# Optimization experiments

Hardware: AMD Instinct MI355X
Metric: run time of the kernel (lower is better)

Reference implementation:

```python
import jax, jax.numpy as jnp
import numpy as np

L = 16
IN0 = 7  # 3 + 3 + 1 per the torch module
CH = [16, 32, 16]
N = 500000
NEG_SLOPE = 0.2


def setup_inputs() -> dict:
    key = jax.random.key(0)
    ks = jax.random.split(key, 5)
    x = jax.random.normal(ks[0], (N, IN0), dtype=jnp.float32)
    idx = jax.random.randint(ks[1], (N,), 0, L, dtype=jnp.int32)
    # kaiming-uniform-like init scale per layer fan-in
    def init_w(k, shape):
        fan_in = shape[1]
        bound = float(np.sqrt(6.0 / fan_in))
        return jax.random.uniform(k, shape, dtype=jnp.float32, minval=-bound, maxval=bound)
    W0 = init_w(ks[2], (L, IN0, CH[0]))
    W1 = init_w(ks[3], (L, CH[0], CH[1]))
    W2 = init_w(ks[4], (L, CH[1], CH[2]))
    b0 = jnp.zeros((L, CH[0]), dtype=jnp.float32)
    b1 = jnp.zeros((L, CH[1]), dtype=jnp.float32)
    b2 = jnp.zeros((L, CH[2]), dtype=jnp.float32)
    return {"x": x, "idx": idx, "W0": W0, "b0": b0, "W1": W1, "b1": b1, "W2": W2, "b2": b2}


def reference(x, idx, W0, b0, W1, b1, W2, b2):
    # Per-point expert-indexed MLP: h <- LeakyReLU(h @ W[idx] + b[idx]) per layer.
    h = x
    for W, b in ((W0, b0), (W1, b1), (W2, b2)):
        # gather per-point weight [N, in, out] and bias [N, out], vec-mat per point
        h = jax.nn.leaky_relu(
            jnp.einsum("nc,nco->no", h, W[idx]) + b[idx],
            negative_slope=NEG_SLOPE,
        )
    return h
```

## Files before the change

kernel.cpp:

```cpp
#include <hip/hip_runtime.h>
#include <hip/hip_fp16.h>


#define L_EXP 16
#define IN0   7
#define C0    16
#define C1    32
#define C2    16
#define NEG   0.2f
#define BLK   256
#define MPT   4
#define SEGPAD (BLK * MPT)
#define CHUNK  1024
#define NBM    512

#define NW0 (L_EXP * IN0 * C0)
#define NW1 (L_EXP * C0 * C1)
#define NW2 (L_EXP * C1 * C2)
#define NWTOT (NW0 + NW1 + NW2)
#define PREPBLK ((NWTOT + BLK - 1) / BLK)

#define WS_PART  64
#define WB_W0    33792
#define WB_W1    37376
#define WB_W2    53760
#define WS_PERM  18432

__global__ void k_hist(const int* __restrict__ idx, int n, int nblk,
                       int* __restrict__ ws,
                       const float* __restrict__ W0,
                       const float* __restrict__ W1,
                       const float* __restrict__ W2) {
    int t = threadIdx.x;
    if (blockIdx.x >= nblk) {
        int k = (blockIdx.x - nblk) * BLK + t;
        __half* hW0 = (__half*)((char*)ws + WB_W0);
        __half* hW1 = (__half*)((char*)ws + WB_W1);
        __half* hW2 = (__half*)((char*)ws + WB_W2);
        if (k < NW0) hW0[k] = __float2half(W0[k]);
        else if (k < NW0 + NW1) hW1[k - NW0] = __float2half(W1[k - NW0]);
        else if (k < NWTOT) hW2[k - NW0 - NW1] = __float2half(W2[k - NW0 - NW1]);
        return;
    }
    __shared__ int bins[L_EXP];
    if (t < L_EXP) bins[t] = 0;
    __syncthreads();
    int i4 = blockIdx.x * CHUNK + t * 4;
    if (i4 + 3 < n) {
        int4 v = *reinterpret_cast<const int4*>(idx + i4);
        atomicAdd(&bins[v.x & 15], 1);
        atomicAdd(&bins[v.y & 15], 1);
        atomicAdd(&bins[v.z & 15], 1);
        atomicAdd(&bins[v.w & 15], 1);
    } else {
#pragma unroll
        for (int q = 0; q < 4; ++q)
            if (i4 + q < n) atomicAdd(&bins[idx[i4 + q] & 15], 1);
    }
    __syncthreads();
    if (t < L_EXP) ws[WS_PART + t * NBM + blockIdx.x] = bins[t];
}

__global__ void k_scan(int* __restrict__ ws, int nblk) {
    int t = threadIdx.x;
    int e = t >> 6, l = t & 63;
    int running = 0;
    for (int c = 0; c < nblk; c += 64) {
        int b = c + l;
        int v = (b < nblk) ? ws[WS_PART + e * NBM + b] : 0;
        int s = v;
#pragma unroll
        for (int d = 1; d < 64; d <<= 1) {
            int u = __shfl_up(s, d, 64);
            if (l >= d) s += u;
        }
        if (b < nblk) ws[WS_PART + e * NBM + b] = running + (s - v);
        running += __shfl(s, 63, 64);
    }
    if (l == 0) ws[e] = running;
    __syncthreads();
    if (t == 0) {
        int run = 0;
        for (int q = 0; q < L_EXP; ++q) {
            ws[16 + q] = run;
            run += ((ws[q] + SEGPAD - 1) / SEGPAD) * SEGPAD;
        }
        ws[32] = run;
    }
}

__global__ void k_scatter(const int* __restrict__ idx, int n,
                          int* __restrict__ ws) {
    __shared__ int soff[L_EXP];
    __shared__ int lcount[L_EXP];
    int t = threadIdx.x;
    if (t < L_EXP) {
        soff[t] = ws[16 + t] + ws[WS_PART + t * NBM + blockIdx.x];
        lcount[t] = 0;
    }
    __syncthreads();
    int i4 = blockIdx.x * CHUNK + t * 4;
#pragma unroll
    for (int q = 0; q < 4; ++q) {
        int i = i4 + q;
        if (i < n) {
            int e = idx[i] & 15;
            int r = atomicAdd(&lcount[e], 1);
            ws[WS_PERM + soff[e] + r] = i;
        }
    }
}

__device__ __forceinline__ float leaky(float a) { return fmaxf(a, NEG * a); }

__device__ __forceinline__ void h8_unpack(float4 v, float* w) {
    const __half2* p = reinterpret_cast<const __half2*>(&v);
    float2 f0 = __half22float2(p[0]);
    float2 f1 = __half22float2(p[1]);
    float2 f2 = __half22float2(p[2]);
    float2 f3 = __half22float2(p[3]);
    w[0] = f0.x; w[1] = f0.y; w[2] = f1.x; w[3] = f1.y;
    w[4] = f2.x; w[5] = f2.y; w[6] = f3.x; w[7] = f3.y;
}

__global__ void __launch_bounds__(BLK, 2) k_mlp(
    const int* __restrict__ meta, const float* __restrict__ x,
    const float* __restrict__ b0, const float* __restrict__ b1,
    const float* __restrict__ b2, float* __restrict__ out) {
    __shared__ __align__(16) __half sW0h[IN0 * C0];
    __shared__ __align__(16) __half sW1h[C0 * C1];
    __shared__ __align__(16) __half sW2h[C1 * C2];
    __shared__ __align__(16) float sB0[C0];
    __shared__ __align__(16) float sB1[C1];
    __shared__ __align__(16) float sB2[C2];

    int start = blockIdx.x * SEGPAD;
    if (start >= meta[32]) return;

    int e = 0;
    while (start >= meta[16 + e + 1]) ++e;
    e = __builtin_amdgcn_readfirstlane(e);

    int t = threadIdx.x;
    {
        const __half* hW0 = (const __half*)((const char*)meta + WB_W0) + e * (IN0 * C0);
        const __half* hW1 = (const __half*)((const char*)meta + WB_W1) + e * (C0 * C1);
        const __half* hW2 = (const __half*)((const char*)meta + WB_W2) + e * (C1 * C2);
        if (t < IN0 * C0) sW0h[t] = hW0[t];
        reinterpret_cast<ushort2*>(sW1h)[t] = reinterpret_cast<const ushort2*>(hW1)[t];
        reinterpret_cast<ushort2*>(sW2h)[t] = reinterpret_cast<const ushort2*>(hW2)[t];
        if (t >= 128 && t < 128 + C0) sB0[t - 128] = b0[e * C0 + (t - 128)];
        if (t >= 160 && t < 160 + C1) sB1[t - 160] = b1[e * C1 + (t - 160)];
        if (t >= 192 && t < 192 + C2) sB2[t - 192] = b2[e * C2 + (t - 192)];
    }
    __syncthreads();

    int seg = meta[16 + e];
    int cnt = meta[e];
    int j0 = start - seg + t;

    float xv[MPT][IN0];
    int   pid[MPT];
    bool  act[MPT];
#pragma unroll
    for (int m = 0; m < MPT; ++m) {
        int j = j0 + m * BLK;
        act[m] = (j < cnt);
        int p = meta[WS_PERM + seg + j];
        pid[m] = act[m] ? p : 0;
        const float* xp = x + (size_t)pid[m] * IN0;
        float4 a = *reinterpret_cast<const float4*>(xp);
        float4 b = *reinterpret_cast<const float4*>(xp + 3);
        xv[m][0] = a.x; xv[m][1] = a.y; xv[m][2] = a.z; xv[m][3] = a.w;
        xv[m][4] = b.y; xv[m][5] = b.z; xv[m][6] = b.w;
    }
    __builtin_amdgcn_sched_barrier(0);

    float h0[MPT][C0];
#pragma unroll
    for (int m = 0; m < MPT; ++m)
#pragma unroll
        for (int o = 0; o < C0; ++o) h0[m][o] = sB0[o];
#pragma unroll
    for (int c = 0; c < IN0; ++c) {
        float w[16];
        h8_unpack(reinterpret_cast<const float4*>(&sW0h[c * C0])[0], w);
        h8_unpack(reinterpret_cast<const float4*>(&sW0h[c * C0])[1], w + 8);
#pragma unroll
        for (int m = 0; m < MPT; ++m)
#pragma unroll
            for (int o = 0; o < C0; ++o) h0[m][o] = fmaf(xv[m][c], w[o], h0[m][o]);
        if (c == 3) __builtin_amdgcn_sched_barrier(0);
    }
#pragma unroll
    for (int m = 0; m < MPT; ++m)
#pragma unroll
        for (int o = 0; o < C0; ++o) h0[m][o] = leaky(h0[m][o]);
    __builtin_amdgcn_sched_barrier(0);

    float h2[MPT][C2];
#pragma unroll
    for (int m = 0; m < MPT; ++m)
#pragma unroll
        for (int o = 0; o < C2; ++o) h2[m][o] = sB2[o];
#pragma unroll 1
    for (int ch = 0; ch < C1 / 8; ++ch) {
        float tv[MPT][8];
#pragma unroll
        for (int m = 0; m < MPT; ++m)
#pragma unroll
            for (int o = 0; o < 8; ++o) tv[m][o] = sB1[ch * 8 + o];
#pragma unroll
        for (int c = 0; c < C0; ++c) {
            float w[8];
            h8_unpack(*reinterpret_cast<const float4*>(&sW1h[c * C1 + ch * 8]), w);
#pragma unroll
            for (int m = 0; m < MPT; ++m)
#pragma unroll
                for (int o = 0; o < 8; ++o) tv[m][o] = fmaf(h0[m][c], w[o], tv[m][o]);
        }
#pragma unroll
        for (int m = 0; m < MPT; ++m)
#pragma unroll
            for (int o = 0; o < 8; ++o) tv[m][o] = leaky(tv[m][o]);
        __builtin_amdgcn_sched_barrier(0);
#pragma unroll
        for (int q = 0; q < 8; ++q) {
            int c1 = ch * 8 + q;
            float w[16];
            h8_unpack(reinterpret_cast<const float4*>(&sW2h[c1 * C2])[0], w);
            h8_unpack(reinterpret_cast<const float4*>(&sW2h[c1 * C2])[1], w + 8);
#pragma unroll
            for (int m = 0; m < MPT; ++m)
#pragma unroll
                for (int o = 0; o < C2; ++o) h2[m][o] = fmaf(tv[m][q], w[o], h2[m][o]);
        }
        __builtin_amdgcn_sched_barrier(0);
    }

#pragma unroll
    for (int m = 0; m < MPT; ++m) {
        if (act[m]) {
            float4* outp = reinterpret_cast<float4*>(out + (size_t)pid[m] * C2);
#pragma unroll
            for (int og = 0; og < C2 / 4; ++og) {
                float4 o;
                o.x = leaky(h2[m][og * 4 + 0]);
                o.y = leaky(h2[m][og * 4 + 1]);
                o.z = leaky(h2[m][og * 4 + 2]);
                o.w = leaky(h2[m][og * 4 + 3]);
                outp[og] = o;
            }
        }
    }
}

extern "C" void kernel_launch(void* const* d_in, const int* in_sizes, int n_in,
                              void* d_out, int out_size, void* d_ws, size_t ws_size,
                              hipStream_t stream) {
    const float* x  = (const float*)d_in[0];
    const int*  idx = (const int*)d_in[1];
    const float* W0 = (const float*)d_in[2];
    const float* b0 = (const float*)d_in[3];
    const float* W1 = (const float*)d_in[4];
    const float* b1 = (const float*)d_in[5];
    const float* W2 = (const float*)d_in[6];
    const float* b2 = (const float*)d_in[7];
    float* out = (float*)d_out;

    int n = in_sizes[1];
    int* ws = (int*)d_ws;

    int nblk = (n + CHUNK - 1) / CHUNK;
    k_hist<<<nblk + PREPBLK, BLK, 0, stream>>>(idx, n, nblk, ws, W0, W1, W2);
    k_scan<<<1, 1024, 0, stream>>>(ws, nblk);
    k_scatter<<<nblk, BLK, 0, stream>>>(idx, n, ws);

    int mblk = (n + L_EXP * (SEGPAD - 1) + SEGPAD - 1) / SEGPAD;
    k_mlp<<<mblk, BLK, 0, stream>>>(ws, x, b0, b1, b2, out);
}
```

Measured before the change: 118.9 us.

## Use packed fp16 dot2 with transposed weights for per-expert MLP

```diff
diff --git a/kernel.cpp b/kernel.cpp
--- a/kernel.cpp
+++ b/kernel.cpp
@@ -14,17 +14,24 @@
 #define CHUNK  1024
 #define NBM    512
 
-#define NW0 (L_EXP * IN0 * C0)
-#define NW1 (L_EXP * C0 * C1)
-#define NW2 (L_EXP * C1 * C2)
-#define NWTOT (NW0 + NW1 + NW2)
-#define PREPBLK ((NWTOT + BLK - 1) / BLK)
+#define NW0T 2048
+#define NW1T 8192
+#define NW2T 8192
+#define NWT_TOT (NW0T + NW1T + NW2T)
+#define PREPBLK (NWT_TOT / BLK)
 
 #define WS_PART  64
-#define WB_W0    33792
-#define WB_W1    37376
-#define WB_W2    53760
+#define WB_W0T   33792
+#define WB_W1T   37888
+#define WB_W2T   54272
 #define WS_PERM  18432
+
+typedef _Float16 h2 __attribute__((ext_vector_type(2)));
+union F4H { float4 f4; h2 h[4]; };
+
+__device__ __forceinline__ h2 pk(float a, float b) {
+    return __builtin_bit_cast(h2, __builtin_amdgcn_cvt_pkrtz(a, b));
+}
 
 __global__ void k_hist(const int* __restrict__ idx, int n, int nblk,
                        int* __restrict__ ws,
@@ -34,12 +41,22 @@
     int t = threadIdx.x;
     if (blockIdx.x >= nblk) {
         int k = (blockIdx.x - nblk) * BLK + t;
-        __half* hW0 = (__half*)((char*)ws + WB_W0);
-        __half* hW1 = (__half*)((char*)ws + WB_W1);
-        __half* hW2 = (__half*)((char*)ws + WB_W2);
-        if (k < NW0) hW0[k] = __float2half(W0[k]);
-        else if (k < NW0 + NW1) hW1[k - NW0] = __float2half(W1[k - NW0]);
-        else if (k < NWTOT) hW2[k - NW0 - NW1] = __float2half(W2[k - NW0 - NW1]);
+        __half* hW0 = (__half*)((char*)ws + WB_W0T);
+        __half* hW1 = (__half*)((char*)ws + WB_W1T);
+        __half* hW2 = (__half*)((char*)ws + WB_W2T);
+        if (k < NW0T) {
+            int e = k >> 7, r = k & 127, o = r >> 3, c = r & 7;
+            float v = (c < IN0) ? W0[e * (IN0 * C0) + c * C0 + o] : 0.0f;
+            hW0[k] = __float2half(v);
+        } else if (k < NW0T + NW1T) {
+            int k2 = k - NW0T;
+            int e = k2 >> 9, r = k2 & 511, o = r >> 4, c = r & 15;
+            hW1[k2] = __float2half(W1[e * (C0 * C1) + c * C1 + o]);
+        } else {
+            int k2 = k - NW0T - NW1T;
+            int e = k2 >> 9, r = k2 & 511, o = r >> 5, c = r & 31;
+            hW2[k2] = __float2half(W2[e * (C1 * C2) + c * C2 + o]);
+        }
         return;
     }
     __shared__ int bins[L_EXP];
@@ -113,23 +130,17 @@
 
 __device__ __forceinline__ float leaky(float a) { return fmaxf(a, NEG * a); }
 
-__device__ __forceinline__ void h8_unpack(float4 v, float* w) {
-    const __half2* p = reinterpret_cast<const __half2*>(&v);
-    float2 f0 = __half22float2(p[0]);
-    float2 f1 = __half22float2(p[1]);
-    float2 f2 = __half22float2(p[2]);
-    float2 f3 = __half22float2(p[3]);
-    w[0] = f0.x; w[1] = f0.y; w[2] = f1.x; w[3] = f1.y;
-    w[4] = f2.x; w[5] = f2.y; w[6] = f3.x; w[7] = f3.y;
+__device__ __forceinline__ float fdot2(h2 a, h2 b, float c) {
+    return __builtin_amdgcn_fdot2(a, b, c, false);
 }
 
 __global__ void __launch_bounds__(BLK, 2) k_mlp(
     const int* __restrict__ meta, const float* __restrict__ x,
     const float* __restrict__ b0, const float* __restrict__ b1,
     const float* __restrict__ b2, float* __restrict__ out) {
-    __shared__ __align__(16) __half sW0h[IN0 * C0];
-    __shared__ __align__(16) __half sW1h[C0 * C1];
-    __shared__ __align__(16) __half sW2h[C1 * C2];
+    __shared__ __align__(16) __half sW0t[C0 * 8];
+    __shared__ __align__(16) __half sW1t[C1 * C0];
+    __shared__ __align__(16) __half sW2t[C2 * C1];
     __shared__ __align__(16) float sB0[C0];
     __shared__ __align__(16) float sB1[C1];
     __shared__ __align__(16) float sB2[C2];
@@ -143,12 +154,12 @@
 
     int t = threadIdx.x;
     {
-        const __half* hW0 = (const __half*)((const char*)meta + WB_W0) + e * (IN0 * C0);
-        const __half* hW1 = (const __half*)((const char*)meta + WB_W1) + e * (C0 * C1);
-        const __half* hW2 = (const __half*)((const char*)meta + WB_W2) + e * (C1 * C2);
-        if (t < IN0 * C0) sW0h[t] = hW0[t];
-        reinterpret_cast<ushort2*>(sW1h)[t] = reinterpret_cast<const ushort2*>(hW1)[t];
-        reinterpret_cast<ushort2*>(sW2h)[t] = reinterpret_cast<const ushort2*>(hW2)[t];
+        const int* w0i = (const int*)((const char*)meta + WB_W0T) + e * 64;
+        const int* w1i = (const int*)((const char*)meta + WB_W1T) + e * 256;
+        const int* w2i = (const int*)((const char*)meta + WB_W2T) + e * 256;
+        if (t < 64) reinterpret_cast<int*>(sW0t)[t] = w0i[t];
+        reinterpret_cast<int*>(sW1t)[t] = w1i[t];
+        reinterpret_cast<int*>(sW2t)[t] = w2i[t];
         if (t >= 128 && t < 128 + C0) sB0[t - 128] = b0[e * C0 + (t - 128)];
         if (t >= 160 && t < 160 + C1) sB1[t - 160] = b1[e * C1 + (t - 160)];
         if (t >= 192 && t < 192 + C2) sB2[t - 192] = b2[e * C2 + (t - 192)];
@@ -159,9 +170,9 @@
     int cnt = meta[e];
     int j0 = start - seg + t;
 
-    float xv[MPT][IN0];
-    int   pid[MPT];
-    bool  act[MPT];
+    h2  xh[MPT][4];
+    int pid[MPT];
+    bool act[MPT];
 #pragma unroll
     for (int m = 0; m < MPT; ++m) {
         int j = j0 + m * BLK;
@@ -171,69 +182,85 @@
         const float* xp = x + (size_t)pid[m] * IN0;
         float4 a = *reinterpret_cast<const float4*>(xp);
         float4 b = *reinterpret_cast<const float4*>(xp + 3);
-        xv[m][0] = a.x; xv[m][1] = a.y; xv[m][2] = a.z; xv[m][3] = a.w;
-        xv[m][4] = b.y; xv[m][5] = b.z; xv[m][6] = b.w;
+        xh[m][0] = pk(a.x, a.y);
+        xh[m][1] = pk(a.z, a.w);
+        xh[m][2] = pk(b.y, b.z);
+        xh[m][3] = pk(b.w, 0.0f);
     }
     __builtin_amdgcn_sched_barrier(0);
 
-    float h0[MPT][C0];
+    float h0f[MPT][C0];
+#pragma unroll
+    for (int o = 0; o < C0; ++o) {
+        F4H u;
+        u.f4 = *reinterpret_cast<const float4*>(&sW0t[o * 8]);
+#pragma unroll
+        for (int m = 0; m < MPT; ++m) {
+            float a = sB0[o];
+            a = fdot2(xh[m][0], u.h[0], a);
+            a = fdot2(xh[m][1], u.h[1], a);
+            a = fdot2(xh[m][2], u.h[2], a);
+            a = fdot2(xh[m][3], u.h[3], a);
+            h0f[m][o] = leaky(a);
+        }
+        if (o == 7) __builtin_amdgcn_sched_barrier(0);
+    }
+    h2 h0h[MPT][8];
 #pragma unroll
     for (int m = 0; m < MPT; ++m)
 #pragma unroll
-        for (int o = 0; o < C0; ++o) h0[m][o] = sB0[o];
-#pragma unroll
-    for (int c = 0; c < IN0; ++c) {
-        float w[16];
-        h8_unpack(reinterpret_cast<const float4*>(&sW0h[c * C0])[0], w);
-        h8_unpack(reinterpret_cast<const float4*>(&sW0h[c * C0])[1], w + 8);
-#pragma unroll
-        for (int m = 0; m < MPT; ++m)
-#pragma unroll
-            for (int o = 0; o < C0; ++o) h0[m][o] = fmaf(xv[m][c], w[o], h0[m][o]);
-        if (c == 3) __builtin_amdgcn_sched_barrier(0);
-    }
+        for (int p = 0; p < 8; ++p)
+            h0h[m][p] = pk(h0f[m][2 * p], h0f[m][2 * p + 1]);
+    __builtin_amdgcn_sched_barrier(0);
+
+    float h2a[MPT][C2];
 #pragma unroll
     for (int m = 0; m < MPT; ++m)
 #pragma unroll
-        for (int o = 0; o < C0; ++o) h0[m][o] = leaky(h0[m][o]);
-    __builtin_amdgcn_sched_barrier(0);
-
-    float h2[MPT][C2];
-#pragma unroll
-    for (int m = 0; m < MPT; ++m)
-#pragma unroll
-        for (int o = 0; o < C2; ++o) h2[m][o] = sB2[o];
+        for (int o = 0; o < C2; ++o) h2a[m][o] = sB2[o];
 #pragma unroll 1
     for (int ch = 0; ch < C1 / 8; ++ch) {
-        float tv[MPT][8];
+        float tvf[MPT][8];
+#pragma unroll
+        for (int o8 = 0; o8 < 8; ++o8) {
+            int o = ch * 8 + o8;
+            F4H ua, ub;
+            ua.f4 = reinterpret_cast<const float4*>(&sW1t[o * C0])[0];
+            ub.f4 = reinterpret_cast<const float4*>(&sW1t[o * C0])[1];
+#pragma unroll
+            for (int m = 0; m < MPT; ++m) {
+                float a = sB1[o];
+                a = fdot2(h0h[m][0], ua.h[0], a);
+                a = fdot2(h0h[m][1], ua.h[1], a);
+                a = fdot2(h0h[m][2], ua.h[2], a);
+                a = fdot2(h0h[m][3], ua.h[3], a);
+                a = fdot2(h0h[m][4], ub.h[0], a);
+                a = fdot2(h0h[m][5], ub.h[1], a);
+                a = fdot2(h0h[m][6], ub.h[2], a);
+                a = fdot2(h0h[m][7], ub.h[3], a);
+                tvf[m][o8] = leaky(a);
+            }
+        }
+        __builtin_amdgcn_sched_barrier(0);
+        h2 tvh[MPT][4];
 #pragma unroll
         for (int m = 0; m < MPT; ++m)
 #pragma unroll
-            for (int o = 0; o < 8; ++o) tv[m][o] = sB1[ch * 8 + o];
-#pragma unroll
-        for (int c = 0; c < C0; ++c) {
-            float w[8];
-            h8_unpack(*reinterpret_cast<const float4*>(&sW1h[c * C1 + ch * 8]), w);
-#pragma unroll
-            for (int m = 0; m < MPT; ++m)
-#pragma unroll
-                for (int o = 0; o < 8; ++o) tv[m][o] = fmaf(h0[m][c], w[o], tv[m][o]);
-        }
-#pragma unroll
-        for (int m = 0; m < MPT; ++m)
-#pragma unroll
-            for (int o = 0; o < 8; ++o) tv[m][o] = leaky(tv[m][o]);
-        __builtin_amdgcn_sched_barrier(0);
-#pragma unroll
-        for (int q = 0; q < 8; ++q) {
-            int c1 = ch * 8 + q;
-            float w[16];
-            h8_unpack(reinterpret_cast<const float4*>(&sW2h[c1 * C2])[0], w);
-            h8_unpack(reinterpret_cast<const float4*>(&sW2h[c1 * C2])[1], w + 8);
-#pragma unroll
-            for (int m = 0; m < MPT; ++m)
-#pragma unroll
-                for (int o = 0; o < C2; ++o) h2[m][o] = fmaf(tv[m][q], w[o], h2[m][o]);
+            for (int p = 0; p < 4; ++p)
+                tvh[m][p] = pk(tvf[m][2 * p], tvf[m][2 * p + 1]);
+#pragma unroll
+        for (int o = 0; o < C2; ++o) {
+            F4H u;
+            u.f4 = *reinterpret_cast<const float4*>(&sW2t[o * C1 + ch * 8]);
+#pragma unroll
+            for (int m = 0; m < MPT; ++m) {
+                float a = h2a[m][o];
+                a = fdot2(tvh[m][0], u.h[0], a);
+                a = fdot2(tvh[m][1], u.h[1], a);
+                a = fdot2(tvh[m][2], u.h[2], a);
+                a = fdot2(tvh[m][3], u.h[3], a);
+                h2a[m][o] = a;
+            }
         }
         __builtin_amdgcn_sched_barrier(0);
     }
@@ -245,10 +272,10 @@
 #pragma unroll
             for (int og = 0; og < C2 / 4; ++og) {
                 float4 o;
-                o.x = leaky(h2[m][og * 4 + 0]);
-                o.y = leaky(h2[m][og * 4 + 1]);
-                o.z = leaky(h2[m][og * 4 + 2]);
-                o.w = leaky(h2[m][og * 4 + 3]);
+                o.x = leaky(h2a[m][og * 4 + 0]);
+                o.y = leaky(h2a[m][og * 4 + 1]);
+                o.z = leaky(h2a[m][og * 4 + 2]);
+                o.w = leaky(h2a[m][og * 4 + 3]);
                 outp[og] = o;
             }
         }
```

After: 117.6 us. Within noise of the previous version (-1.1%).
